# Kernel tuning notes

Hardware: AMD Instinct MI355X
Metric: run time of the kernel (lower is better)

Reference implementation:

```python
import jax, jax.numpy as jnp
import numpy as np

B, T, E = 2, 4096, 1024
H = 16
D = E // H  # head_len = 64


def setup_inputs() -> dict:
    key = jax.random.key(0)
    ks = jax.random.split(key, 6)
    s = 1.0 / np.sqrt(E)
    return {
        "x": jax.random.normal(ks[0], (B, T, E), dtype=jnp.float32),
        # torch nn.Linear weights: shape (out, in), y = x @ W.T
        "Wq": jax.random.uniform(ks[1], (E, E), jnp.float32, -s, s),
        "Wk": jax.random.uniform(ks[2], (E, E), jnp.float32, -s, s),
        "Wv": jax.random.uniform(ks[3], (E, E), jnp.float32, -s, s),
        "Wo": jax.random.uniform(ks[4], (E, E), jnp.float32, -s, s),
        "bo": jax.random.uniform(ks[5], (E,), jnp.float32, -s, s),
    }


def reference(x, Wq, Wk, Wv, Wo, bo):
    Bx, Tx, Ex = x.shape
    q = x @ Wq.T
    k = x @ Wk.T
    v = x @ Wv.T
    # (B, T, H, D) -> (B, H, T, D)
    q = q.reshape(Bx, Tx, H, D).transpose(0, 2, 1, 3)
    k = k.reshape(Bx, Tx, H, D).transpose(0, 2, 1, 3)
    v = v.reshape(Bx, Tx, H, D).transpose(0, 2, 1, 3)
    # scores: (B, H, T, T), scaled by sqrt(head_len)
    sim = jnp.einsum("bhqd,bhkd->bhqk", q, k) / jnp.sqrt(jnp.float32(D))
    causal = jnp.tril(jnp.ones((Tx, Tx), dtype=bool))  # True = keep
    sim = jnp.where(causal[None, None], sim, -jnp.inf)
    attn = jax.nn.softmax(sim, axis=-1)
    # dropout_rate = 0.0 (eval) -> identity
    out = jnp.einsum("bhqk,bhkd->bhqd", attn, v)
    out = out.transpose(0, 2, 1, 3).reshape(Bx, Tx, Ex)
    return out @ Wo.T + bo
```

## Files before the change

kernel.cpp:

```cpp
#include <hip/hip_runtime.h>

typedef unsigned short bf16_t;
typedef __bf16 bf16x8 __attribute__((ext_vector_type(8)));
typedef float  v4f   __attribute__((ext_vector_type(4)));
typedef float  v16f  __attribute__((ext_vector_type(16)));
typedef unsigned u32x2 __attribute__((ext_vector_type(2)));

__device__ __forceinline__ bf16_t f2bf(float f) {
    union { float f; unsigned u; } a; a.f = f;
    unsigned r = a.u + 0x7FFFu + ((a.u >> 16) & 1u);
    return (bf16_t)(r >> 16);
}

__device__ __forceinline__ unsigned cvtpk(float lo, float hi) {
    unsigned r;
    asm("v_cvt_pk_bf16_f32 %0, %1, %2" : "=v"(r) : "v"(lo), "v"(hi));
    return r;
}

__device__ __forceinline__ v16f zero16() {
    v16f z;
#pragma unroll
    for (int i = 0; i < 16; ++i) z[i] = 0.f;
    return z;
}

#define GL16(g, l) __builtin_amdgcn_global_load_lds( \
    (__attribute__((address_space(1))) void*)(g),    \
    (__attribute__((address_space(3))) void*)(l), 16, 0, 0)

#define QSCALE 0.18033688011f

__global__ __launch_bounds__(256) void cvt_all(
    const float4* __restrict__ x,  const float4* __restrict__ wq,
    const float4* __restrict__ wk, const float4* __restrict__ wv,
    const float4* __restrict__ wo,
    ushort4* __restrict__ xb, ushort4* __restrict__ wqkv, ushort4* __restrict__ wob) {
    int i = blockIdx.x * 256 + threadIdx.x;
    const float4* s; ushort4* d; int off;
    if (i < 2097152) { s = x; d = xb; off = i; }
    else {
        int wdx = (i - 2097152) >> 18;
        off = (i - 2097152) & 262143;
        if      (wdx == 0) { s = wq; d = wqkv; }
        else if (wdx == 1) { s = wk; d = wqkv + 262144; }
        else if (wdx == 2) { s = wv; d = wqkv + 524288; }
        else               { s = wo; d = wob; }
    }
    float4 v = s[off];
    ushort4 o;
    o.x = f2bf(v.x); o.y = f2bf(v.y); o.z = f2bf(v.z); o.w = f2bf(v.w);
    d[off] = o;
}

#define GEMM_MAINLOOP(A_, W_)                                                          \
    __shared__ bf16_t SMEM[8192];                                                      \
    bf16_t* As = SMEM; bf16_t* Bs = SMEM + 4096;                                       \
    const int tid = threadIdx.x;                                                       \
    const int w = tid >> 6, lane = tid & 63;                                           \
    const int lrow = lane & 15, lq = lane >> 4;                                        \
    const int nwg_ = gridDim.x * gridDim.y;                                            \
    const int id_ = blockIdx.y * gridDim.x + blockIdx.x;                               \
    const int sid_ = (id_ & 7) * (nwg_ >> 3) + (id_ >> 3);                             \
    const int bxs = sid_ % gridDim.x, bys = sid_ / gridDim.x;                          \
    const int m0 = bys * 128, n0 = bxs * 128;                                          \
    const int srow = w * 16 + (lane >> 2);                                             \
    const int sk = (lane & 3) * 8;                                                     \
    const int wm = (w & 1) * 64, wn = (w >> 1) * 64;                                   \
    v4f acc[4][4];                                                                     \
    _Pragma("unroll") for (int i = 0; i < 4; ++i)                                      \
        _Pragma("unroll") for (int j = 0; j < 4; ++j)                                  \
            acc[i][j] = (v4f){0.f, 0.f, 0.f, 0.f};                                     \
    for (int k0 = 0; k0 < 1024; k0 += 32) {                                            \
        __syncthreads();                                                               \
        GL16(A_ + (size_t)(m0 + srow) * 1024 + k0 + sk,      (char*)As + w * 1024);    \
        GL16(A_ + (size_t)(m0 + 64 + srow) * 1024 + k0 + sk, (char*)As + 4096 + w * 1024); \
        GL16(W_ + (size_t)(n0 + srow) * 1024 + k0 + sk,      (char*)Bs + w * 1024);    \
        GL16(W_ + (size_t)(n0 + 64 + srow) * 1024 + k0 + sk, (char*)Bs + 4096 + w * 1024); \
        __syncthreads();                                                               \
        bf16x8 af[4], bf[4];                                                           \
        _Pragma("unroll") for (int i = 0; i < 4; ++i)                                  \
            af[i] = *(const bf16x8*)&As[(wm + i * 16 + lrow) * 32 + lq * 8];           \
        _Pragma("unroll") for (int j = 0; j < 4; ++j)                                  \
            bf[j] = *(const bf16x8*)&Bs[(wn + j * 16 + lrow) * 32 + lq * 8];           \
        _Pragma("unroll") for (int i = 0; i < 4; ++i)                                  \
            _Pragma("unroll") for (int j = 0; j < 4; ++j)                              \
                acc[i][j] = __builtin_amdgcn_mfma_f32_16x16x32_bf16(af[i], bf[j],      \
                                                                    acc[i][j], 0, 0, 0); \
    }

__global__ __launch_bounds__(256) void gemm_qkv_kernel(
    const bf16_t* __restrict__ A, const bf16_t* __restrict__ W,
    bf16_t* __restrict__ Qb, bf16_t* __restrict__ Kb, bf16_t* __restrict__ Vtb) {
    GEMM_MAINLOOP(A, W)
    const int x = bxs;
    const int b = m0 >> 12, t0 = m0 & 4095;
    if (x < 8) {
#pragma unroll
        for (int i = 0; i < 4; ++i)
#pragma unroll
            for (int j = 0; j < 4; ++j)
#pragma unroll
                for (int r = 0; r < 4; ++r) {
                    int t = t0 + wm + i * 16 + lq * 4 + r;
                    int n = n0 + wn + j * 16 + lrow;
                    int h = n >> 6, d = n & 63;
                    Qb[(((size_t)b * 16 + h) * 4096 + t) * 64 + d] =
                        f2bf(acc[i][j][r] * QSCALE);
                }
    } else if (x < 16) {
#pragma unroll
        for (int i = 0; i < 4; ++i)
#pragma unroll
            for (int j = 0; j < 4; ++j)
#pragma unroll
                for (int r = 0; r < 4; ++r) {
                    int t = t0 + wm + i * 16 + lq * 4 + r;
                    int nn = n0 + wn + j * 16 + lrow - 1024;
                    int h = nn >> 6, d = nn & 63;
                    Kb[(((size_t)b * 16 + h) * 4096 + t) * 64 + d] = f2bf(acc[i][j][r]);
                }
    } else {
        const int d0 = n0 - 2048;
#pragma unroll 1
        for (int p = 0; p < 2; ++p) {
            __syncthreads();
            if ((w >> 1) == p) {
#pragma unroll
                for (int i = 0; i < 4; ++i)
#pragma unroll
                    for (int j = 0; j < 4; ++j) {
                        int row = j * 16 + lrow;
                        int swz = (row & 7) << 1;
                        int g = (wm >> 2) + i * 4 + lq;
                        uint2 u;
                        u.x = (unsigned)f2bf(acc[i][j][0]) | ((unsigned)f2bf(acc[i][j][1]) << 16);
                        u.y = (unsigned)f2bf(acc[i][j][2]) | ((unsigned)f2bf(acc[i][j][3]) << 16);
                        *(uint2*)&SMEM[row * 128 + ((g ^ swz) << 2)] = u;
                    }
            }
            __syncthreads();
#pragma unroll
            for (int uu = 0; uu < 4; ++uu) {
                int unit = tid + 256 * uu;
                int row = unit >> 4, seg = unit & 15;
                uint4 val = *(const uint4*)&SMEM[row * 128 + ((seg ^ (row & 7)) << 3)];
                *(uint4*)&Vtb[((size_t)b * 1024 + d0 + p * 64 + row) * 4096 + t0 + seg * 8] = val;
            }
        }
    }
}

__global__ __launch_bounds__(256) void gemm_out_kernel(
    const bf16_t* __restrict__ A, const bf16_t* __restrict__ W,
    const float* __restrict__ bo, float* __restrict__ out) {
    GEMM_MAINLOOP(A, W)
#pragma unroll
    for (int j = 0; j < 4; ++j) {
        int n = n0 + wn + j * 16 + lrow;
        float bias = bo[n];
#pragma unroll
        for (int i = 0; i < 4; ++i)
#pragma unroll
            for (int r = 0; r < 4; ++r) {
                int m = m0 + wm + i * 16 + lq * 4 + r;
                out[(size_t)m * 1024 + n] = acc[i][j][r] + bias;
            }
    }
}

__global__ __launch_bounds__(256, 2) void attn_kernel(
    const bf16_t* __restrict__ Q, const bf16_t* __restrict__ K,
    const bf16_t* __restrict__ Vt, bf16_t* __restrict__ O) {
    __shared__ bf16_t Kls[2][64 * 64];
    __shared__ bf16_t Vls[2][64 * 64];
    const int tid = threadIdx.x;
    const int w = tid >> 6, lane = tid & 63;
    const int l31 = lane & 31, lh = lane >> 5;

    const int id = blockIdx.y * 16 + blockIdx.x;
    const int g = (id >> 3) & 15;
    const int bh = (id & 7) + ((id >> 7) << 3);

    const bf16_t* Qh = Q + (size_t)bh * (4096 * 64);
    const bf16_t* Kh = K + (size_t)bh * (4096 * 64);
    const bf16_t* Vh = Vt + (size_t)bh * (64 * 4096);
    const int b = bh >> 4, h = bh & 15;

    const int svrow = lane >> 3;
    const int sg8 = ((lane & 7) ^ svrow) * 8;
    const int rx = l31 & 7;

    bf16x8 ones;
#pragma unroll
    for (int i = 0; i < 8; ++i) ones[i] = (__bf16)1.0f;

#pragma unroll 1
    for (int mem = 0; mem < 2; ++mem) {
        const int j = mem ? (31 - g) : g;
        const int q0 = j * 128;
        const int q0w = q0 + w * 32;
        const int nt = 2 * j + 2;
        const int wlast = 2 * j + (w >> 1);
        const int qglob = q0w + l31;

        bf16x8 qf[4];
#pragma unroll
        for (int dk = 0; dk < 4; ++dk)
            qf[dk] = *(const bf16x8*)&Qh[(size_t)(q0w + l31) * 64 + dk * 16 + lh * 8];

        v16f oacc0 = zero16(), oacc1 = zero16(), lacc = zero16();

        auto stage = [&](int kt, int buf) {
            const int kc0 = kt << 6;
#pragma unroll
            for (int i = 0; i < 2; ++i) {
                int r0 = w * 16 + i * 8;
                GL16(Kh + (size_t)(kc0 + r0 + svrow) * 64 + sg8, (char*)&Kls[buf][r0 * 64]);
                GL16(Vh + (size_t)(r0 + svrow) * 4096 + kc0 + sg8, (char*)&Vls[buf][r0 * 64]);
            }
        };

        stage(0, 0);
        for (int kt = 0; kt < nt; ++kt) {
            const int buf = kt & 1;
            __syncthreads();
            if (kt + 1 < nt) stage(kt + 1, buf ^ 1);
            if (kt > wlast) continue;
            const int kc0 = kt << 6;
            const bool diag = (kt == wlast);

            bf16x8 kf[2][4];
#pragma unroll
            for (int th = 0; th < 2; ++th)
#pragma unroll
                for (int dk = 0; dk < 4; ++dk)
                    kf[th][dk] = *(const bf16x8*)
                        &Kls[buf][(th * 32 + l31) * 64 + (((dk * 2 + lh) ^ rx) * 8)];
            bf16x8 vf[2][4];
#pragma unroll
            for (int db = 0; db < 2; ++db)
#pragma unroll
                for (int kb = 0; kb < 4; ++kb)
                    vf[db][kb] = *(const bf16x8*)
                        &Vls[buf][(db * 32 + l31) * 64 + (((kb * 2 + lh) ^ rx) * 8)];

            v16f st0 = zero16(), st1 = zero16();
#pragma unroll
            for (int dk = 0; dk < 4; ++dk) {
                st0 = __builtin_amdgcn_mfma_f32_32x32x16_bf16(kf[0][dk], qf[dk], st0, 0, 0, 0);
                st1 = __builtin_amdgcn_mfma_f32_32x32x16_bf16(kf[1][dk], qf[dk], st1, 0, 0, 0);
            }

            bf16x8 pa[4];
#pragma unroll
            for (int th = 0; th < 2; ++th) {
                float p[16];
#pragma unroll
                for (int rr = 0; rr < 16; ++rr) {
                    float pv = __builtin_amdgcn_exp2f(th ? st1[rr] : st0[rr]);
                    if (diag) {
                        int tg = kc0 + th * 32 + (rr & 3) + 8 * (rr >> 2) + 4 * lh;
                        pv = (tg > qglob) ? 0.f : pv;
                    }
                    p[rr] = pv;
                }
#pragma unroll
                for (int kb2 = 0; kb2 < 2; ++kb2) {
                    unsigned x0 = cvtpk(p[kb2 * 8 + 0], p[kb2 * 8 + 1]);
                    unsigned x1 = cvtpk(p[kb2 * 8 + 2], p[kb2 * 8 + 3]);
                    unsigned y0 = cvtpk(p[kb2 * 8 + 4], p[kb2 * 8 + 5]);
                    unsigned y1 = cvtpk(p[kb2 * 8 + 6], p[kb2 * 8 + 7]);
                    u32x2 ra = __builtin_amdgcn_permlane32_swap(x0, y0, false, false);
                    u32x2 rb = __builtin_amdgcn_permlane32_swap(x1, y1, false, false);
                    union { unsigned u[4]; bf16x8 v; } pu;
                    pu.u[0] = ra.x; pu.u[1] = rb.x;
                    pu.u[2] = ra.y; pu.u[3] = rb.y;
                    pa[th * 2 + kb2] = pu.v;
                }
            }

#pragma unroll
            for (int kb = 0; kb < 4; ++kb) {
                lacc  = __builtin_amdgcn_mfma_f32_32x32x16_bf16(pa[kb], ones,       lacc,  0, 0, 0);
                oacc0 = __builtin_amdgcn_mfma_f32_32x32x16_bf16(pa[kb], vf[0][kb], oacc0, 0, 0, 0);
                oacc1 = __builtin_amdgcn_mfma_f32_32x32x16_bf16(pa[kb], vf[1][kb], oacc1, 0, 0, 0);
            }
        }

#pragma unroll
        for (int rr = 0; rr < 16; ++rr) {
            float rl = 1.0f / lacc[rr];
            int q = q0w + (rr & 3) + 8 * (rr >> 2) + 4 * lh;
            size_t o0 = ((size_t)b * 4096 + q) * 1024 + h * 64;
            O[o0 + l31]      = f2bf(oacc0[rr] * rl);
            O[o0 + 32 + l31] = f2bf(oacc1[rr] * rl);
        }
    }
}

extern "C" void kernel_launch(void* const* d_in, const int* in_sizes, int n_in,
                              void* d_out, int out_size, void* d_ws, size_t ws_size,
                              hipStream_t stream) {
    const float* x  = (const float*)d_in[0];
    const float* Wq = (const float*)d_in[1];
    const float* Wk = (const float*)d_in[2];
    const float* Wv = (const float*)d_in[3];
    const float* Wo = (const float*)d_in[4];
    const float* bo = (const float*)d_in[5];
    float* out = (float*)d_out;

    char* ws = (char*)d_ws;
    bf16_t* xb   = (bf16_t*)(ws + 0);
    bf16_t* Wqkv = (bf16_t*)(ws + 16777216);
    bf16_t* Wob  = (bf16_t*)(ws + 23068672);
    bf16_t* Qb   = (bf16_t*)(ws + 25165824);
    bf16_t* Kb   = (bf16_t*)(ws + 41943040);
    bf16_t* Vtb  = (bf16_t*)(ws + 58720256);
    bf16_t* Ob   = (bf16_t*)(ws + 75497472);

    cvt_all<<<12288, 256, 0, stream>>>((const float4*)x, (const float4*)Wq,
                                       (const float4*)Wk, (const float4*)Wv,
                                       (const float4*)Wo,
                                       (ushort4*)xb, (ushort4*)Wqkv, (ushort4*)Wob);

    gemm_qkv_kernel<<<dim3(24, 64), 256, 0, stream>>>(xb, Wqkv, Qb, Kb, Vtb);

    attn_kernel<<<dim3(16, 32), 256, 0, stream>>>(Qb, Kb, Vtb, Ob);

    gemm_out_kernel<<<dim3(8, 64), 256, 0, stream>>>(Ob, Wob, bo, out);
}
```

Measured before the change: 295.4 us.

## Enlarge QKV GEMM tile to 256x128 with 512 threads and XCD-aware mapping

The QKV projection GEMM now runs with 512-thread blocks that each compute a 256x128 tile instead of 128x128, halving the grid along M. Block IDs are remapped so each XCD works on a contiguous group of M rows, improving L2 reuse of the A rows. The larger tile reduces how often weight tiles are reloaded per output. In exchange it uses more LDS per block and fewer blocks (768), which may lower occupancy and change how the tail of the grid fills the GPU.

Result: no change. 290.9 us (-1.5%).

```diff
diff --git a/kernel.cpp b/kernel.cpp
--- a/kernel.cpp
+++ b/kernel.cpp
@@ -51,6 +51,113 @@
     ushort4 o;
     o.x = f2bf(v.x); o.y = f2bf(v.y); o.z = f2bf(v.z); o.w = f2bf(v.w);
     d[off] = o;
+}
+
+__global__ __launch_bounds__(512, 4) void gemm_qkv_kernel(
+    const bf16_t* __restrict__ A, const bf16_t* __restrict__ W,
+    bf16_t* __restrict__ Qb, bf16_t* __restrict__ Kb, bf16_t* __restrict__ Vtb) {
+    __shared__ bf16_t SMEM[16384];
+    bf16_t* As = SMEM;
+    bf16_t* Bs = SMEM + 8192;
+    const int tid = threadIdx.x;
+    const int w = tid >> 6, lane = tid & 63;
+    const int lrow = lane & 15, lq = lane >> 4;
+    const int id_ = blockIdx.y * 24 + blockIdx.x;
+    const int xcd_ = id_ & 7, r_ = id_ >> 3;
+    const int bys = xcd_ * 4 + (r_ & 3), bxs = r_ >> 2;
+    const int m0 = bys * 256, n0 = bxs * 128;
+    const int srw = lane >> 2;
+    const int sk = (lane & 3) * 8;
+    const int wm = (w & 3) * 64, wn = (w >> 2) * 64;
+    v4f acc[4][4];
+#pragma unroll
+    for (int i = 0; i < 4; ++i)
+#pragma unroll
+        for (int j = 0; j < 4; ++j) acc[i][j] = (v4f){0.f, 0.f, 0.f, 0.f};
+
+    for (int k0 = 0; k0 < 1024; k0 += 32) {
+        __syncthreads();
+#pragma unroll
+        for (int c = 0; c < 3; ++c) {
+            int u = w * 3 + c;
+            if (u < 16)
+                GL16(A + (size_t)(m0 + u * 16 + srw) * 1024 + k0 + sk, (char*)As + u * 1024);
+            else
+                GL16(W + (size_t)(n0 + (u - 16) * 16 + srw) * 1024 + k0 + sk,
+                     (char*)Bs + (u - 16) * 1024);
+        }
+        __syncthreads();
+        bf16x8 af[4], bf[4];
+#pragma unroll
+        for (int i = 0; i < 4; ++i)
+            af[i] = *(const bf16x8*)&As[(wm + i * 16 + lrow) * 32 + lq * 8];
+#pragma unroll
+        for (int j = 0; j < 4; ++j)
+            bf[j] = *(const bf16x8*)&Bs[(wn + j * 16 + lrow) * 32 + lq * 8];
+#pragma unroll
+        for (int i = 0; i < 4; ++i)
+#pragma unroll
+            for (int j = 0; j < 4; ++j)
+                acc[i][j] = __builtin_amdgcn_mfma_f32_16x16x32_bf16(af[i], bf[j],
+                                                                    acc[i][j], 0, 0, 0);
+    }
+
+    const int x = bxs;
+    const int b = m0 >> 12, t0 = m0 & 4095;
+    if (x < 8) {
+#pragma unroll
+        for (int i = 0; i < 4; ++i)
+#pragma unroll
+            for (int j = 0; j < 4; ++j)
+#pragma unroll
+                for (int r = 0; r < 4; ++r) {
+                    int t = t0 + wm + i * 16 + lq * 4 + r;
+                    int n = n0 + wn + j * 16 + lrow;
+                    int h = n >> 6, d = n & 63;
+                    Qb[(((size_t)b * 16 + h) * 4096 + t) * 64 + d] =
+                        f2bf(acc[i][j][r] * QSCALE);
+                }
+    } else if (x < 16) {
+#pragma unroll
+        for (int i = 0; i < 4; ++i)
+#pragma unroll
+            for (int j = 0; j < 4; ++j)
+#pragma unroll
+                for (int r = 0; r < 4; ++r) {
+                    int t = t0 + wm + i * 16 + lq * 4 + r;
+                    int nn = n0 + wn + j * 16 + lrow - 1024;
+                    int h = nn >> 6, d = nn & 63;
+                    Kb[(((size_t)b * 16 + h) * 4096 + t) * 64 + d] = f2bf(acc[i][j][r]);
+                }
+    } else {
+        const int d0 = n0 - 2048;
+#pragma unroll 1
+        for (int p = 0; p < 2; ++p) {
+            __syncthreads();
+            if ((w >> 2) == p) {
+#pragma unroll
+                for (int i = 0; i < 4; ++i)
+#pragma unroll
+                    for (int j = 0; j < 4; ++j) {
+                        int row = j * 16 + lrow;
+                        int swz = (row & 7) << 1;
+                        int g = (wm >> 2) + i * 4 + lq;
+                        uint2 u;
+                        u.x = (unsigned)f2bf(acc[i][j][0]) | ((unsigned)f2bf(acc[i][j][1]) << 16);
+                        u.y = (unsigned)f2bf(acc[i][j][2]) | ((unsigned)f2bf(acc[i][j][3]) << 16);
+                        *(uint2*)&SMEM[row * 256 + ((g ^ swz) << 2)] = u;
+                    }
+            }
+            __syncthreads();
+#pragma unroll
+            for (int uu = 0; uu < 4; ++uu) {
+                int unit = tid + 512 * uu;
+                int row = unit >> 5, seg = unit & 31;
+                uint4 val = *(const uint4*)&SMEM[row * 256 + ((seg ^ (row & 7)) << 3)];
+                *(uint4*)&Vtb[((size_t)b * 1024 + d0 + p * 64 + row) * 4096 + t0 + seg * 8] = val;
+            }
+        }
+    }
 }
 
 #define GEMM_MAINLOOP(A_, W_)                                                          \
@@ -89,68 +196,6 @@
                                                                     acc[i][j], 0, 0, 0); \
     }
 
-__global__ __launch_bounds__(256) void gemm_qkv_kernel(
-    const bf16_t* __restrict__ A, const bf16_t* __restrict__ W,
-    bf16_t* __restrict__ Qb, bf16_t* __restrict__ Kb, bf16_t* __restrict__ Vtb) {
-    GEMM_MAINLOOP(A, W)
-    const int x = bxs;
-    const int b = m0 >> 12, t0 = m0 & 4095;
-    if (x < 8) {
-#pragma unroll
-        for (int i = 0; i < 4; ++i)
-#pragma unroll
-            for (int j = 0; j < 4; ++j)
-#pragma unroll
-                for (int r = 0; r < 4; ++r) {
-                    int t = t0 + wm + i * 16 + lq * 4 + r;
-                    int n = n0 + wn + j * 16 + lrow;
-                    int h = n >> 6, d = n & 63;
-                    Qb[(((size_t)b * 16 + h) * 4096 + t) * 64 + d] =
-                        f2bf(acc[i][j][r] * QSCALE);
-                }
-    } else if (x < 16) {
-#pragma unroll
-        for (int i = 0; i < 4; ++i)
-#pragma unroll
-            for (int j = 0; j < 4; ++j)
-#pragma unroll
-                for (int r = 0; r < 4; ++r) {
-                    int t = t0 + wm + i * 16 + lq * 4 + r;
-                    int nn = n0 + wn + j * 16 + lrow - 1024;
-                    int h = nn >> 6, d = nn & 63;
-                    Kb[(((size_t)b * 16 + h) * 4096 + t) * 64 + d] = f2bf(acc[i][j][r]);
-                }
-    } else {
-        const int d0 = n0 - 2048;
-#pragma unroll 1
-        for (int p = 0; p < 2; ++p) {
-            __syncthreads();
-            if ((w >> 1) == p) {
-#pragma unroll
-                for (int i = 0; i < 4; ++i)
-#pragma unroll
-                    for (int j = 0; j < 4; ++j) {
-                        int row = j * 16 + lrow;
-                        int swz = (row & 7) << 1;
-                        int g = (wm >> 2) + i * 4 + lq;
-                        uint2 u;
-                        u.x = (unsigned)f2bf(acc[i][j][0]) | ((unsigned)f2bf(acc[i][j][1]) << 16);
-                        u.y = (unsigned)f2bf(acc[i][j][2]) | ((unsigned)f2bf(acc[i][j][3]) << 16);
-                        *(uint2*)&SMEM[row * 128 + ((g ^ swz) << 2)] = u;
-                    }
-            }
-            __syncthreads();
-#pragma unroll
-            for (int uu = 0; uu < 4; ++uu) {
-                int unit = tid + 256 * uu;
-                int row = unit >> 4, seg = unit & 15;
-                uint4 val = *(const uint4*)&SMEM[row * 128 + ((seg ^ (row & 7)) << 3)];
-                *(uint4*)&Vtb[((size_t)b * 1024 + d0 + p * 64 + row) * 4096 + t0 + seg * 8] = val;
-            }
-        }
-    }
-}
-
 __global__ __launch_bounds__(256) void gemm_out_kernel(
     const bf16_t* __restrict__ A, const bf16_t* __restrict__ W,
     const float* __restrict__ bo, float* __restrict__ out) {
@@ -324,7 +369,7 @@
                                        (const float4*)Wo,
                                        (ushort4*)xb, (ushort4*)Wqkv, (ushort4*)Wob);
 
-    gemm_qkv_kernel<<<dim3(24, 64), 256, 0, stream>>>(xb, Wqkv, Qb, Kb, Vtb);
+    gemm_qkv_kernel<<<dim3(24, 32), 512, 0, stream>>>(xb, Wqkv, Qb, Kb, Vtb);
 
     attn_kernel<<<dim3(16, 32), 256, 0, stream>>>(Qb, Kb, Vtb, Ob);
 
```
